# Performance work log

Measured on AMD Instinct MI355X. Metric: run time of the kernel, lower is better.

The kernel has to match this reference:

```python
import jax, jax.numpy as jnp
import numpy as np

NUM_CLASSES = 80
TOPK = 100
EPS = 1e-6


def _conv(x, w, b, pad):
    y = jax.lax.conv_general_dilated(
        x, w, window_strides=(1, 1), padding=[(pad, pad), (pad, pad)],
        dimension_numbers=('NCHW', 'OIHW', 'NCHW'))
    return y + b[None, :, None, None]


def _seek_local_maximum(p):
    # 8-neighbor local-maximum test with zero padding, plus >= EPS threshold.
    pp = jnp.pad(p, ((0, 0), (0, 0), (1, 1), (1, 1)))
    m = ((p >= pp[:, :, :-2, 1:-1]) & (p >= pp[:, :, 2:, 1:-1]) &
         (p >= pp[:, :, 1:-1, :-2]) & (p >= pp[:, :, 1:-1, 2:]) &
         (p >= pp[:, :, :-2, :-2]) & (p >= pp[:, :, :-2, 2:]) &
         (p >= pp[:, :, 2:, :-2]) & (p >= pp[:, :, 2:, 2:]) &
         (p >= EPS))
    return m.astype(p.dtype)


def setup_inputs() -> dict:
    key = jax.random.key(0)
    k = jax.random.split(key, 4)
    B, C, H, W = 8, 256, 128, 128
    return {
        'x': jax.random.normal(k[0], (B, C, H, W), jnp.float32),
        'pos_embeddings': jax.random.normal(k[1], (1, C, H, W), jnp.float32),
        'w1': jax.random.normal(k[2], (C, C, 3, 3), jnp.float32) * 0.02,
        'b1': jnp.zeros((C,), jnp.float32),
        'w2': jax.random.normal(k[3], (NUM_CLASSES + 1, C, 1, 1), jnp.float32) * 0.02,
        'b2': jnp.zeros((NUM_CLASSES + 1,), jnp.float32),
    }


def reference(x, pos_embeddings, w1, b1, w2, b2):
    b, c, h, w = x.shape
    # conv3x3 -> relu -> conv1x1 class logits  [b, num_classes+1, h, w]
    logits = _conv(jax.nn.relu(_conv(x, w1, b1, 1)), w2, b2, 0)
    probs = jax.nn.softmax(logits, axis=1)
    # keep only the winning foreground class per pixel (one-hot mask)
    cls_idx = jnp.argmax(probs[:, :NUM_CLASSES], axis=1)  # [b, h, w]
    one_hot = jax.nn.one_hot(cls_idx, NUM_CLASSES + 1, dtype=probs.dtype)
    probs = probs * jnp.transpose(one_hot, (0, 3, 1, 2))
    # boost local maxima (unrolled NMS) then topk over best-class score map
    probs = probs + _seek_local_maximum(probs)
    scores = jnp.max(probs[:, :NUM_CLASSES], axis=1).reshape(b, h * w)
    _, idx = jax.lax.top_k(scores, TOPK)  # [b, TOPK]
    topk_proposals = jnp.take_along_axis(
        x.reshape(b, c, h * w), idx[:, None, :], axis=2)
    pe = jnp.broadcast_to(pos_embeddings, (b,) + pos_embeddings.shape[1:])
    topk_pos_embeddings = jnp.take_along_axis(
        pe.reshape(b, -1, h * w), idx[:, None, :], axis=2)
    # eval mode: topk_locations is None in the original; omit it here
    return topk_proposals, topk_pos_embeddings, logits
```

## Files before the change

kernel.cpp:

```cpp
#include <hip/hip_runtime.h>
#include <cmath>

#define BATCH 8
#define CHN 256
#define HH 128
#define WW 128
#define HWSZ (HH*WW)
#define NCLS 81
#define NFG 80
#define KTOP 100
#define EPSV 1e-6f

typedef __attribute__((ext_vector_type(8))) short short8;
typedef __attribute__((ext_vector_type(4))) float f32x4;

__device__ __forceinline__ ushort f2bf(float f) {
    unsigned u = __float_as_uint(f);
    return (ushort)((u + 0x7FFFu + ((u >> 16) & 1u)) >> 16);
}
__device__ __forceinline__ float bf2f(ushort h) {
    return __uint_as_float(((unsigned)h) << 16);
}

__device__ __forceinline__ void gl16(const void* g, void* l) {
    __builtin_amdgcn_global_load_lds(
        (const __attribute__((address_space(1))) void*)g,
        (__attribute__((address_space(3))) void*)l, 16, 0, 0);
}

__global__ __launch_bounds__(256) void prep_x(
    const float* __restrict__ x, ushort* __restrict__ xh, ushort* __restrict__ xl)
{
    __shared__ float tile[32][CHN + 1];
    const int blk = blockIdx.x;
    const int q4 = blk & 3, h = (blk >> 2) & 127, b = blk >> 9;
    const int w0 = q4 << 5;
    const int t = threadIdx.x;
    const int px1 = t & 31, cq = t >> 5;

    const float* xb = x + ((size_t)b * CHN) * HWSZ + h * WW + w0;
#pragma unroll 4
    for (int i = 0; i < 32; ++i) {
        int c = i * 8 + cq;
        tile[px1][c] = xb[(size_t)c * HWSZ + px1];
    }
    __syncthreads();
    for (int i = 0; i < 4; ++i) {
        int u = i * 256 + t;
        int c8 = u & 31, px = u >> 5;
        short8 hv, lv;
#pragma unroll
        for (int j = 0; j < 8; ++j) {
            float f = tile[px][c8 * 8 + j];
            ushort hb = f2bf(f);
            hv[j] = (short)hb;
            lv[j] = (short)f2bf(f - bf2f(hb));
        }
        size_t addr = ((size_t)b * HWSZ + h * WW + w0 + px) * CHN + c8 * 8;
        *(short8*)(xh + addr) = hv;
        *(short8*)(xl + addr) = lv;
    }
}

__global__ __launch_bounds__(256) void prep_w(
    const float* __restrict__ w1, const float* __restrict__ w2,
    ushort* __restrict__ Bsw, ushort* __restrict__ w2sw)
{
    int i = blockIdx.x * 256 + threadIdx.x;
    if (i < 73728) {
        int tap  = i >> 13;
        int rem  = i & 8191;
        int kt   = rem >> 10;
        int rem2 = rem & 1023;
        int ntg  = rem2 >> 6;
        int lane = rem2 & 63;
        int oc   = ntg * 16 + (lane & 15);
        int ic0  = kt * 32 + (lane >> 4) * 8;
        size_t base = (size_t)(tap * 8 + kt) * 16384 + (size_t)ntg * 512 + lane * 8;
#pragma unroll
        for (int j = 0; j < 8; ++j) {
            float w  = w1[(size_t)oc * 2304 + (ic0 + j) * 9 + tap];
            ushort hb = f2bf(w);
            Bsw[base + j]        = hb;
            Bsw[base + 8192 + j] = f2bf(w - bf2f(hb));
        }
    } else {
        int j2 = i - 73728;
        int kt   = j2 / 768;
        int rem  = j2 - kt * 768;
        int spl  = rem / 384;
        int rem2 = rem - spl * 384;
        int ntg  = rem2 >> 6;
        int lane = rem2 & 63;
        int oc   = ntg * 16 + (lane & 15);
        int ic0  = kt * 32 + (lane >> 4) * 8;
        size_t base = (size_t)(kt * 12 + spl * 6 + ntg) * 512 + lane * 8;
#pragma unroll
        for (int j = 0; j < 8; ++j) {
            float w = (oc < NCLS) ? w2[(size_t)oc * CHN + ic0 + j] : 0.f;
            ushort hb = f2bf(w);
            w2sw[base + j] = spl ? f2bf(w - bf2f(hb)) : hb;
        }
    }
}

__global__ __launch_bounds__(256, 2) void conv3_pipe(
    const ushort* __restrict__ xh, const ushort* __restrict__ xl,
    const ushort* __restrict__ Bsw, const float* __restrict__ b1,
    float* __restrict__ y)
{
    __shared__ ushort A[3][2][132 * 32];

    const int blk  = blockIdx.x;
    const int b    = blk & 7;
    const int h    = blk >> 3;
    const int t    = threadIdx.x;
    const int lane = t & 63;
    const int w    = t >> 6;
    const int l15  = lane & 15;
    const int q    = lane >> 4;

    int colb[4], ldsu[4], basew[4];
#pragma unroll
    for (int r = 0; r < 4; ++r) {
        int e   = (r * 256 + t) & 511;
        int pxs = (e >> 2) + 1;
        int qq  = e & 3;
        int qs  = qq ^ ((pxs >> 1) & 3);
        colb[r]  = (pxs - 1) * CHN + qs * 8;
        ldsu[r]  = pxs * 32 + qq * 8;
        basew[r] = ((((r * 256 + (t & 192)) & 511) >> 2) + 1) * 32;
    }

    const short8 zz = {0, 0, 0, 0, 0, 0, 0, 0};
    f32x4 acc[8][4];
#pragma unroll
    for (int i = 0; i < 8; ++i)
#pragma unroll
        for (int j = 0; j < 4; ++j) { f32x4 z = {0.f, 0.f, 0.f, 0.f}; acc[i][j] = z; }

    if (t < 96) {
        int sl = t >> 5, rr = t & 31, arr = rr >> 4, pp = (rr >> 2) & 3, qq = rr & 3;
        int pxs = pp ? 128 + pp : 0;
        *(short8*)&A[sl][arr][pxs * 32 + qq * 8] = zz;
    }

    auto stage = [&](int sn) {
        int kt1 = sn / 3;
        int kh1 = sn - kt1 * 3;
        int gh  = h - 1 + kh1;
        if ((unsigned)gh < (unsigned)HH) {
            size_t rowb = ((size_t)(b * HH + gh) * WW) * CHN + kt1 * 32;
#pragma unroll
            for (int r = 0; r < 4; ++r) {
                const ushort* g = (r < 2 ? xh : xl) + rowb + colb[r];
                gl16(g, &A[kh1][r >> 1][basew[r]]);
            }
        } else {
#pragma unroll
            for (int r = 0; r < 4; ++r)
                *(short8*)&A[kh1][r >> 1][ldsu[r]] = zz;
        }
    };

    stage(0);
    __syncthreads();

#pragma unroll 1
    for (int s = 0; s < 24; ++s) {
        const int kt = s / 3;
        const int kh = s - kt * 3;
#pragma unroll
        for (int kw = 0; kw < 3; ++kw) {
            const int tap = kh * 3 + kw;
            const ushort* bk = Bsw + (size_t)(tap * 8 + kt) * 16384 + lane * 8;
            short8 bh[4], bl[4];
#pragma unroll
            for (int nt = 0; nt < 4; ++nt) {
                bh[nt] = *(const short8*)(bk + (w * 4 + nt) * 512);
                bl[nt] = *(const short8*)(bk + 8192 + (w * 4 + nt) * 512);
            }
            if (kw == 0 && s < 23) stage(s + 1);
#pragma unroll
            for (int mth = 0; mth < 8; mth += 4) {
                short8 ahf[4], alf[4];
#pragma unroll
                for (int mm = 0; mm < 4; ++mm) {
                    int pxs = (mth + mm) * 16 + l15 + kw;
                    int cof = pxs * 32 + ((q ^ ((pxs >> 1) & 3)) * 8);
                    ahf[mm] = *(const short8*)&A[kh][0][cof];
                    alf[mm] = *(const short8*)&A[kh][1][cof];
                }
                __builtin_amdgcn_s_setprio(1);
#pragma unroll
                for (int nt = 0; nt < 4; ++nt) {
#pragma unroll
                    for (int mm = 0; mm < 4; ++mm)
                        acc[mth + mm][nt] = __builtin_amdgcn_mfma_f32_16x16x32_bf16(
                            ahf[mm], bh[nt], acc[mth + mm][nt], 0, 0, 0);
#pragma unroll
                    for (int mm = 0; mm < 4; ++mm)
                        acc[mth + mm][nt] = __builtin_amdgcn_mfma_f32_16x16x32_bf16(
                            ahf[mm], bl[nt], acc[mth + mm][nt], 0, 0, 0);
#pragma unroll
                    for (int mm = 0; mm < 4; ++mm)
                        acc[mth + mm][nt] = __builtin_amdgcn_mfma_f32_16x16x32_bf16(
                            alf[mm], bh[nt], acc[mth + mm][nt], 0, 0, 0);
                }
                __builtin_amdgcn_s_setprio(0);
            }
        }
        __syncthreads();
    }

    const size_t rowbase = (size_t)b * HWSZ + h * WW;
#pragma unroll
    for (int nt = 0; nt < 4; ++nt) {
        const int oc = w * 64 + nt * 16 + l15;
        const float bias = b1[oc];
#pragma unroll
        for (int mt = 0; mt < 8; ++mt) {
#pragma unroll
            for (int r = 0; r < 4; ++r) {
                const int px = mt * 16 + q * 4 + r;
                float v = acc[mt][nt][r] + bias;
                y[(rowbase + px) * CHN + oc] = v > 0.f ? v : 0.f;
            }
        }
    }
}

__global__ __launch_bounds__(256) void head_mfma(
    const float* __restrict__ y, const ushort* __restrict__ w2sw,
    const float* __restrict__ b2, float* __restrict__ logits_out,
    int* __restrict__ cls_map, float* __restrict__ prob_map)
{
    __shared__ float ls[128][97];
    const int blk = blockIdx.x;
    const int b = blk >> 7, h = blk & 127;
    const int t = threadIdx.x, lane = t & 63, wm = t >> 6;
    const int l15 = lane & 15, q = lane >> 4;

    f32x4 acc[2][6];
#pragma unroll
    for (int i = 0; i < 2; ++i)
#pragma unroll
        for (int j = 0; j < 6; ++j) { f32x4 z = {0.f, 0.f, 0.f, 0.f}; acc[i][j] = z; }

    const size_t rowbase = (size_t)b * HWSZ + h * WW;

    for (int kt = 0; kt < 8; ++kt) {
        short8 ah[2], al[2];
#pragma unroll
        for (int mt = 0; mt < 2; ++mt) {
            const float* src = y + (rowbase + wm * 32 + mt * 16 + l15) * CHN + kt * 32 + q * 8;
            float4 f0 = *(const float4*)src;
            float4 f1 = *(const float4*)(src + 4);
            float fv[8] = {f0.x, f0.y, f0.z, f0.w, f1.x, f1.y, f1.z, f1.w};
#pragma unroll
            for (int j = 0; j < 8; ++j) {
                ushort hb = f2bf(fv[j]);
                ah[mt][j] = (short)hb;
                al[mt][j] = (short)f2bf(fv[j] - bf2f(hb));
            }
        }
        const ushort* bk = w2sw + (size_t)kt * 12 * 512 + lane * 8;
#pragma unroll
        for (int nt = 0; nt < 6; ++nt) {
            short8 bh = *(const short8*)(bk + nt * 512);
            short8 bl = *(const short8*)(bk + (6 + nt) * 512);
#pragma unroll
            for (int mt = 0; mt < 2; ++mt) {
                acc[mt][nt] = __builtin_amdgcn_mfma_f32_16x16x32_bf16(ah[mt], bh, acc[mt][nt], 0, 0, 0);
                acc[mt][nt] = __builtin_amdgcn_mfma_f32_16x16x32_bf16(ah[mt], bl, acc[mt][nt], 0, 0, 0);
                acc[mt][nt] = __builtin_amdgcn_mfma_f32_16x16x32_bf16(al[mt], bh, acc[mt][nt], 0, 0, 0);
            }
        }
    }

#pragma unroll
    for (int nt = 0; nt < 6; ++nt) {
        const int oc = nt * 16 + l15;
        const float bias = (oc < NCLS) ? b2[oc] : 0.f;
#pragma unroll
        for (int mt = 0; mt < 2; ++mt) {
#pragma unroll
            for (int r = 0; r < 4; ++r) {
                const int px = wm * 32 + mt * 16 + q * 4 + r;
                ls[px][oc] = acc[mt][nt][r] + bias;
            }
        }
    }
    __syncthreads();

    for (int i = t; i < NCLS * 128; i += 256) {
        int c = i >> 7, px = i & 127;
        logits_out[((size_t)b * NCLS + c) * HWSZ + h * WW + px] = ls[px][c];
    }

    if (t < 128) {
        const int px = t;
        float m = -1e30f;
#pragma unroll
        for (int c = 0; c < NCLS; ++c) m = fmaxf(m, ls[px][c]);
        float s = 0.f;
        for (int c = 0; c < NCLS; ++c) s += expf(ls[px][c] - m);
        float best = -1e30f; int bc = 0;
        for (int c = 0; c < NFG; ++c) {
            float v = ls[px][c];
            if (v > best) { best = v; bc = c; }
        }
        cls_map[rowbase + px]  = bc;
        prob_map[rowbase + px] = expf(best - m) / s;
    }
}

__global__ __launch_bounds__(256) void locmax_kernel(
    const int* __restrict__ cls_map, const float* __restrict__ prob_map,
    float* __restrict__ score)
{
    int i = blockIdx.x * 256 + threadIdx.x;
    int b = i >> 14;
    int p = i & (HWSZ - 1);
    int h = p >> 7, w = p & 127;
    int mycls = cls_map[i];
    float myp = prob_map[i];
    bool lm = (myp >= EPSV);
#pragma unroll
    for (int dh = -1; dh <= 1; ++dh)
#pragma unroll
        for (int dw = -1; dw <= 1; ++dw) {
            if (dh == 0 && dw == 0) continue;
            int nh = h + dh, nw = w + dw;
            if ((unsigned)nh < HH && (unsigned)nw < WW) {
                int ni = b * HWSZ + nh * WW + nw;
                if (cls_map[ni] == mycls && myp < prob_map[ni]) lm = false;
            }
        }
    score[i] = myp + (lm ? 1.f : 0.f);
}

__global__ __launch_bounds__(1024) void topk_kernel(
    const float* __restrict__ score, int* __restrict__ idx_out)
{
    __shared__ unsigned int hist[256];
    __shared__ unsigned long long cand[2048];
    __shared__ unsigned int sprefix, sneed, scntA, scntB;
    const int b = blockIdx.x;
    const int t = threadIdx.x;
    const float* sc = score + b * HWSZ;

    unsigned keys[16];
#pragma unroll
    for (int i = 0; i < 16; ++i)
        keys[i] = __float_as_uint(sc[t + (i << 10)]);

    if (t == 0) { sneed = KTOP; sprefix = 0; scntA = 0; scntB = 0; }

    for (int lvl = 0; lvl < 4; ++lvl) {
        const int shift = 24 - 8 * lvl;
        if (t < 256) hist[t] = 0;
        __syncthreads();
        const unsigned pref = sprefix;
#pragma unroll
        for (int i = 0; i < 16; ++i) {
            unsigned k = keys[i];
            bool match = (lvl == 0) || ((k >> (shift + 8)) == pref);
            if (match) atomicAdd(&hist[(k >> shift) & 255u], 1u);
        }
        __syncthreads();
        if (t == 0) {
            unsigned needv = sneed, c = 0; int bsel = 0;
            for (int j = 255; j >= 0; --j) {
                unsigned nc = c + hist[j];
                if (nc >= needv) { bsel = j; break; }
                c = nc;
            }
            sprefix = (pref << 8) | (unsigned)bsel;
            sneed = needv - c;
        }
        __syncthreads();
    }

    const unsigned K = sprefix;
#pragma unroll
    for (int i = 0; i < 16; ++i) {
        unsigned k = keys[i];
        int p = t + (i << 10);
        if (k > K) {
            unsigned pos = atomicAdd(&scntA, 1u);
            cand[pos] = ((unsigned long long)k << 32) | (unsigned)(~p);
        } else if (k == K) {
            unsigned pos = atomicAdd(&scntB, 1u);
            if (pos < 1920u)
                cand[128 + pos] = ((unsigned long long)k << 32) | (unsigned)(~p);
        }
    }
    __syncthreads();
    const int cA = (int)scntA;
    const int cB = (int)(scntB < 1920u ? scntB : 1920u);
    const int Ctot = cA + cB;
    for (int ti = t; ti < Ctot; ti += 1024) {
        unsigned long long my = cand[ti < cA ? ti : 128 + (ti - cA)];
        int rank = 0;
        for (int j = 0; j < Ctot; ++j) {
            unsigned long long o = cand[j < cA ? j : 128 + (j - cA)];
            rank += (o > my) ? 1 : 0;
        }
        if (rank < KTOP)
            idx_out[b * KTOP + rank] =
                (int)(~(unsigned)(my & 0xFFFFFFFFull)) & (HWSZ - 1);
    }
}

__global__ __launch_bounds__(256) void gather_kernel(
    const float* __restrict__ x, const float* __restrict__ pos,
    const int* __restrict__ idx, float* __restrict__ out0,
    float* __restrict__ out1)
{
    int blk = blockIdx.x;
    int b = blk / KTOP;
    int j = blk - b * KTOP;
    int c = threadIdx.x;
    int pix = idx[b * KTOP + j];
    out0[((size_t)b * CHN + c) * KTOP + j] = x[((size_t)b * CHN + c) * HWSZ + pix];
    out1[((size_t)b * CHN + c) * KTOP + j] = pos[(size_t)c * HWSZ + pix];
}

extern "C" void kernel_launch(void* const* d_in, const int* in_sizes, int n_in,
                              void* d_out, int out_size, void* d_ws, size_t ws_size,
                              hipStream_t stream) {
    (void)in_sizes; (void)n_in; (void)out_size; (void)ws_size;
    const float* x   = (const float*)d_in[0];
    const float* pos = (const float*)d_in[1];
    const float* w1  = (const float*)d_in[2];
    const float* b1  = (const float*)d_in[3];
    const float* w2  = (const float*)d_in[4];
    const float* b2  = (const float*)d_in[5];

    float* out0   = (float*)d_out;
    float* out1   = out0 + BATCH * CHN * KTOP;
    float* logits = out1 + BATCH * CHN * KTOP;

    char* ws = (char*)d_ws;
    const size_t NPX = (size_t)BATCH * HWSZ;

    size_t off = 0;
    int*    cls_map  = (int*)(ws + off);    off += NPX * 4;
    float*  prob_map = (float*)(ws + off);  off += NPX * 4;
    float*  score    = (float*)(ws + off);  off += NPX * 4;
    int*    idx      = (int*)(ws + off);    off += 4096;
    ushort* w2sw     = (ushort*)(ws + off); off += (size_t)8 * 12 * 512 * 2;
    ushort* Bsw      = (ushort*)(ws + off); off += (size_t)9 * 8 * 16384 * 2;
    ushort* xh       = (ushort*)(ws + off); off += NPX * CHN * 2;
    ushort* xl       = (ushort*)(ws + off); off += NPX * CHN * 2;
    float*  y        = (float*)(ws + off);  off += NPX * CHN * 4;

    prep_x<<<4096, 256, 0, stream>>>(x, xh, xl);
    prep_w<<<312, 256, 0, stream>>>(w1, w2, Bsw, w2sw);
    conv3_pipe<<<1024, 256, 0, stream>>>(xh, xl, Bsw, b1, y);
    head_mfma<<<1024, 256, 0, stream>>>(y, w2sw, b2, logits, cls_map, prob_map);
    locmax_kernel<<<(int)(NPX / 256), 256, 0, stream>>>(cls_map, prob_map, score);
    topk_kernel<<<BATCH, 1024, 0, stream>>>(score, idx);
    gather_kernel<<<BATCH * KTOP, 256, 0, stream>>>(x, pos, idx, out0, out1);
}
```

Baseline: 716.6 us.

## Fuse 1x1 class head and softmax epilogue into conv3x3 kernel

The conv3x3 kernel no longer writes the full fp32 ReLU activation tensor to global memory. It stages 32-pixel chunks of the accumulators into swizzled shared memory, reusing the input staging buffer through a union, and runs the 1x1 head MFMA, logits store and softmax/argmax there directly. This removes a 128 MB write and read-back plus one kernel launch. In exchange the conv epilogue gets longer, with extra block barriers and a larger LDS footprint that may limit occupancy.

```diff
diff --git a/kernel.cpp b/kernel.cpp
--- a/kernel.cpp
+++ b/kernel.cpp
@@ -26,6 +26,10 @@
     __builtin_amdgcn_global_load_lds(
         (const __attribute__((address_space(1))) void*)g,
         (__attribute__((address_space(3))) void*)l, 16, 0, 0);
+}
+
+__device__ __forceinline__ int ys_idx(int row, int col) {
+    return row * 256 + ((((col >> 2) ^ row) & 15) << 2) + ((col >> 2) & ~15) * 4 + (col & 3);
 }
 
 __global__ __launch_bounds__(256) void prep_x(
@@ -104,12 +108,17 @@
     }
 }
 
-__global__ __launch_bounds__(256, 2) void conv3_pipe(
+__global__ __launch_bounds__(256, 2) void conv3_fused(
     const ushort* __restrict__ xh, const ushort* __restrict__ xl,
     const ushort* __restrict__ Bsw, const float* __restrict__ b1,
-    float* __restrict__ y)
-{
-    __shared__ ushort A[3][2][132 * 32];
+    const ushort* __restrict__ w2sw, const float* __restrict__ b2,
+    float* __restrict__ logits_out, int* __restrict__ cls_map,
+    float* __restrict__ prob_map)
+{
+    __shared__ union SMU {
+        ushort A[3][2][132 * 32];
+        struct { float ys[32 * 256]; float ls[32 * 103]; } ep;
+    } sm;
 
     const int blk  = blockIdx.x;
     const int b    = blk & 7;
@@ -142,7 +151,7 @@
     if (t < 96) {
         int sl = t >> 5, rr = t & 31, arr = rr >> 4, pp = (rr >> 2) & 3, qq = rr & 3;
         int pxs = pp ? 128 + pp : 0;
-        *(short8*)&A[sl][arr][pxs * 32 + qq * 8] = zz;
+        *(short8*)&sm.A[sl][arr][pxs * 32 + qq * 8] = zz;
     }
 
     auto stage = [&](int sn) {
@@ -154,12 +163,12 @@
 #pragma unroll
             for (int r = 0; r < 4; ++r) {
                 const ushort* g = (r < 2 ? xh : xl) + rowb + colb[r];
-                gl16(g, &A[kh1][r >> 1][basew[r]]);
+                gl16(g, &sm.A[kh1][r >> 1][basew[r]]);
             }
         } else {
 #pragma unroll
             for (int r = 0; r < 4; ++r)
-                *(short8*)&A[kh1][r >> 1][ldsu[r]] = zz;
+                *(short8*)&sm.A[kh1][r >> 1][ldsu[r]] = zz;
         }
     };
 
@@ -188,8 +197,8 @@
                 for (int mm = 0; mm < 4; ++mm) {
                     int pxs = (mth + mm) * 16 + l15 + kw;
                     int cof = pxs * 32 + ((q ^ ((pxs >> 1) & 3)) * 8);
-                    ahf[mm] = *(const short8*)&A[kh][0][cof];
-                    alf[mm] = *(const short8*)&A[kh][1][cof];
+                    ahf[mm] = *(const short8*)&sm.A[kh][0][cof];
+                    alf[mm] = *(const short8*)&sm.A[kh][1][cof];
                 }
                 __builtin_amdgcn_s_setprio(1);
 #pragma unroll
@@ -214,104 +223,95 @@
     }
 
     const size_t rowbase = (size_t)b * HWSZ + h * WW;
-#pragma unroll
-    for (int nt = 0; nt < 4; ++nt) {
-        const int oc = w * 64 + nt * 16 + l15;
-        const float bias = b1[oc];
-#pragma unroll
-        for (int mt = 0; mt < 8; ++mt) {
-#pragma unroll
-            for (int r = 0; r < 4; ++r) {
-                const int px = mt * 16 + q * 4 + r;
-                float v = acc[mt][nt][r] + bias;
-                y[(rowbase + px) * CHN + oc] = v > 0.f ? v : 0.f;
-            }
-        }
-    }
-}
-
-__global__ __launch_bounds__(256) void head_mfma(
-    const float* __restrict__ y, const ushort* __restrict__ w2sw,
-    const float* __restrict__ b2, float* __restrict__ logits_out,
-    int* __restrict__ cls_map, float* __restrict__ prob_map)
-{
-    __shared__ float ls[128][97];
-    const int blk = blockIdx.x;
-    const int b = blk >> 7, h = blk & 127;
-    const int t = threadIdx.x, lane = t & 63, wm = t >> 6;
-    const int l15 = lane & 15, q = lane >> 4;
-
-    f32x4 acc[2][6];
-#pragma unroll
-    for (int i = 0; i < 2; ++i)
-#pragma unroll
-        for (int j = 0; j < 6; ++j) { f32x4 z = {0.f, 0.f, 0.f, 0.f}; acc[i][j] = z; }
-
-    const size_t rowbase = (size_t)b * HWSZ + h * WW;
-
-    for (int kt = 0; kt < 8; ++kt) {
-        short8 ah[2], al[2];
-#pragma unroll
-        for (int mt = 0; mt < 2; ++mt) {
-            const float* src = y + (rowbase + wm * 32 + mt * 16 + l15) * CHN + kt * 32 + q * 8;
-            float4 f0 = *(const float4*)src;
-            float4 f1 = *(const float4*)(src + 4);
+    const int mt2sel = w >> 1;
+    const int ntb    = (w & 1) * 3;
+
+    float b1c[4];
+#pragma unroll
+    for (int nt = 0; nt < 4; ++nt) b1c[nt] = b1[w * 64 + nt * 16 + l15];
+    float b2c[3];
+#pragma unroll
+    for (int j = 0; j < 3; ++j) {
+        int oc2 = (ntb + j) * 16 + l15;
+        b2c[j] = (oc2 < NCLS) ? b2[oc2] : 0.f;
+    }
+
+    float* ys = sm.ep.ys;
+    float* ls = sm.ep.ls;
+
+#pragma unroll
+    for (int p = 0; p < 4; ++p) {
+        __syncthreads();
+#pragma unroll
+        for (int h2 = 0; h2 < 2; ++h2) {
+#pragma unroll
+            for (int nt = 0; nt < 4; ++nt) {
+                const int col = w * 64 + nt * 16 + l15;
+#pragma unroll
+                for (int r = 0; r < 4; ++r) {
+                    const int row = h2 * 16 + q * 4 + r;
+                    float v = acc[2 * p + h2][nt][r] + b1c[nt];
+                    ys[ys_idx(row, col)] = v > 0.f ? v : 0.f;
+                }
+            }
+        }
+        __syncthreads();
+        f32x4 acc2[3];
+#pragma unroll
+        for (int j = 0; j < 3; ++j) { f32x4 z = {0.f, 0.f, 0.f, 0.f}; acc2[j] = z; }
+        const int arow = mt2sel * 16 + l15;
+#pragma unroll
+        for (int kt = 0; kt < 8; ++kt) {
+            const int c0 = kt * 32 + q * 8;
+            float4 f0 = *(const float4*)&ys[arow * 256 + ((((c0 >> 2) ^ arow) & 15) << 2) + ((c0 >> 2) & ~15) * 4];
+            const int c1 = c0 + 4;
+            float4 f1 = *(const float4*)&ys[arow * 256 + ((((c1 >> 2) ^ arow) & 15) << 2) + ((c1 >> 2) & ~15) * 4];
             float fv[8] = {f0.x, f0.y, f0.z, f0.w, f1.x, f1.y, f1.z, f1.w};
+            short8 ah, al;
 #pragma unroll
             for (int j = 0; j < 8; ++j) {
                 ushort hb = f2bf(fv[j]);
-                ah[mt][j] = (short)hb;
-                al[mt][j] = (short)f2bf(fv[j] - bf2f(hb));
-            }
-        }
-        const ushort* bk = w2sw + (size_t)kt * 12 * 512 + lane * 8;
-#pragma unroll
-        for (int nt = 0; nt < 6; ++nt) {
-            short8 bh = *(const short8*)(bk + nt * 512);
-            short8 bl = *(const short8*)(bk + (6 + nt) * 512);
-#pragma unroll
-            for (int mt = 0; mt < 2; ++mt) {
-                acc[mt][nt] = __builtin_amdgcn_mfma_f32_16x16x32_bf16(ah[mt], bh, acc[mt][nt], 0, 0, 0);
-                acc[mt][nt] = __builtin_amdgcn_mfma_f32_16x16x32_bf16(ah[mt], bl, acc[mt][nt], 0, 0, 0);
-                acc[mt][nt] = __builtin_amdgcn_mfma_f32_16x16x32_bf16(al[mt], bh, acc[mt][nt], 0, 0, 0);
-            }
-        }
-    }
-
-#pragma unroll
-    for (int nt = 0; nt < 6; ++nt) {
-        const int oc = nt * 16 + l15;
-        const float bias = (oc < NCLS) ? b2[oc] : 0.f;
-#pragma unroll
-        for (int mt = 0; mt < 2; ++mt) {
-#pragma unroll
-            for (int r = 0; r < 4; ++r) {
-                const int px = wm * 32 + mt * 16 + q * 4 + r;
-                ls[px][oc] = acc[mt][nt][r] + bias;
-            }
-        }
-    }
-    __syncthreads();
-
-    for (int i = t; i < NCLS * 128; i += 256) {
-        int c = i >> 7, px = i & 127;
-        logits_out[((size_t)b * NCLS + c) * HWSZ + h * WW + px] = ls[px][c];
-    }
-
-    if (t < 128) {
-        const int px = t;
-        float m = -1e30f;
-#pragma unroll
-        for (int c = 0; c < NCLS; ++c) m = fmaxf(m, ls[px][c]);
-        float s = 0.f;
-        for (int c = 0; c < NCLS; ++c) s += expf(ls[px][c] - m);
-        float best = -1e30f; int bc = 0;
-        for (int c = 0; c < NFG; ++c) {
-            float v = ls[px][c];
-            if (v > best) { best = v; bc = c; }
-        }
-        cls_map[rowbase + px]  = bc;
-        prob_map[rowbase + px] = expf(best - m) / s;
+                ah[j] = (short)hb;
+                al[j] = (short)f2bf(fv[j] - bf2f(hb));
+            }
+            const ushort* bk = w2sw + (size_t)kt * 12 * 512 + lane * 8;
+#pragma unroll
+            for (int j = 0; j < 3; ++j) {
+                const int nt = ntb + j;
+                short8 bh = *(const short8*)(bk + nt * 512);
+                short8 bl = *(const short8*)(bk + (6 + nt) * 512);
+                acc2[j] = __builtin_amdgcn_mfma_f32_16x16x32_bf16(ah, bh, acc2[j], 0, 0, 0);
+                acc2[j] = __builtin_amdgcn_mfma_f32_16x16x32_bf16(ah, bl, acc2[j], 0, 0, 0);
+                acc2[j] = __builtin_amdgcn_mfma_f32_16x16x32_bf16(al, bh, acc2[j], 0, 0, 0);
+            }
+        }
+#pragma unroll
+        for (int j = 0; j < 3; ++j) {
+            const int oc2 = (ntb + j) * 16 + l15;
+#pragma unroll
+            for (int r = 0; r < 4; ++r)
+                ls[(mt2sel * 16 + q * 4 + r) * 103 + oc2] = acc2[j][r] + b2c[j];
+        }
+        __syncthreads();
+        if (t < 32) {
+            const int px = t;
+            float m = -1e30f;
+#pragma unroll
+            for (int c = 0; c < NCLS; ++c) m = fmaxf(m, ls[px * 103 + c]);
+            float s = 0.f;
+            for (int c = 0; c < NCLS; ++c) s += expf(ls[px * 103 + c] - m);
+            float best = -1e30f; int bc = 0;
+            for (int c = 0; c < NFG; ++c) {
+                float v = ls[px * 103 + c];
+                if (v > best) { best = v; bc = c; }
+            }
+            cls_map[rowbase + p * 32 + px]  = bc;
+            prob_map[rowbase + p * 32 + px] = expf(best - m) / s;
+        }
+        for (int i = t; i < NCLS * 32; i += 256) {
+            int c = i >> 5, pxl = i & 31;
+            logits_out[((size_t)b * NCLS + c) * HWSZ + h * WW + p * 32 + pxl] = ls[pxl * 103 + c];
+        }
     }
 }
 
@@ -454,12 +454,11 @@
     ushort* Bsw      = (ushort*)(ws + off); off += (size_t)9 * 8 * 16384 * 2;
     ushort* xh       = (ushort*)(ws + off); off += NPX * CHN * 2;
     ushort* xl       = (ushort*)(ws + off); off += NPX * CHN * 2;
-    float*  y        = (float*)(ws + off);  off += NPX * CHN * 4;
 
     prep_x<<<4096, 256, 0, stream>>>(x, xh, xl);
     prep_w<<<312, 256, 0, stream>>>(w1, w2, Bsw, w2sw);
-    conv3_pipe<<<1024, 256, 0, stream>>>(xh, xl, Bsw, b1, y);
-    head_mfma<<<1024, 256, 0, stream>>>(y, w2sw, b2, logits, cls_map, prob_map);
+    conv3_fused<<<1024, 256, 0, stream>>>(xh, xl, Bsw, b1, w2sw, b2,
+                                          logits, cls_map, prob_map);
     locmax_kernel<<<(int)(NPX / 256), 256, 0, stream>>>(cls_map, prob_map, score);
     topk_kernel<<<BATCH, 1024, 0, stream>>>(score, idx);
     gather_kernel<<<BATCH * KTOP, 256, 0, stream>>>(x, pos, idx, out0, out1);
```

Result: slower. 760.2 us (+6.1%).

## Deepen conv3 staging pipeline, prefetch head inputs, and re-pad transpose tile

Applied to the files above, without the earlier changes.

In the 3x3 conv kernel, input rows are now staged two steps ahead instead of one. The per-step __syncthreads is replaced by an explicit vmcnt wait plus s_barrier, and the boundary-row zero fills move to a one-time prologue. In the head kernel, all y fragments are software-prefetched into registers and refilled ahead of use. The prep_x LDS tile gets a padded layout (stride 10 per 8 channels) to reduce bank conflicts. The hand-written waitcnt counts are fragile and must match the number of async loads issued per stage, and the prefetch buffers add register pressure.

```diff
diff --git a/kernel.cpp b/kernel.cpp
--- a/kernel.cpp
+++ b/kernel.cpp
@@ -31,7 +31,7 @@
 __global__ __launch_bounds__(256) void prep_x(
     const float* __restrict__ x, ushort* __restrict__ xh, ushort* __restrict__ xl)
 {
-    __shared__ float tile[32][CHN + 1];
+    __shared__ float tile[32 * 321];
     const int blk = blockIdx.x;
     const int q4 = blk & 3, h = (blk >> 2) & 127, b = blk >> 9;
     const int w0 = q4 << 5;
@@ -41,8 +41,7 @@
     const float* xb = x + ((size_t)b * CHN) * HWSZ + h * WW + w0;
 #pragma unroll 4
     for (int i = 0; i < 32; ++i) {
-        int c = i * 8 + cq;
-        tile[px1][c] = xb[(size_t)c * HWSZ + px1];
+        tile[px1 * 321 + i * 10 + cq] = xb[(size_t)(i * 8 + cq) * HWSZ + px1];
     }
     __syncthreads();
     for (int i = 0; i < 4; ++i) {
@@ -51,7 +50,7 @@
         short8 hv, lv;
 #pragma unroll
         for (int j = 0; j < 8; ++j) {
-            float f = tile[px][c8 * 8 + j];
+            float f = tile[px * 321 + c8 * 10 + j];
             ushort hb = f2bf(f);
             hv[j] = (short)hb;
             lv[j] = (short)f2bf(f - bf2f(hb));
@@ -120,7 +119,7 @@
     const int l15  = lane & 15;
     const int q    = lane >> 4;
 
-    int colb[4], ldsu[4], basew[4];
+    int colb[4], basew[4];
 #pragma unroll
     for (int r = 0; r < 4; ++r) {
         int e   = (r * 256 + t) & 511;
@@ -128,7 +127,6 @@
         int qq  = e & 3;
         int qs  = qq ^ ((pxs >> 1) & 3);
         colb[r]  = (pxs - 1) * CHN + qs * 8;
-        ldsu[r]  = pxs * 32 + qq * 8;
         basew[r] = ((((r * 256 + (t & 192)) & 511) >> 2) + 1) * 32;
     }
 
@@ -143,6 +141,13 @@
         int sl = t >> 5, rr = t & 31, arr = rr >> 4, pp = (rr >> 2) & 3, qq = rr & 3;
         int pxs = pp ? 128 + pp : 0;
         *(short8*)&A[sl][arr][pxs * 32 + qq * 8] = zz;
+    }
+    if (h == 0 || h == 127) {
+        const int sl = (h == 0) ? 0 : 2;
+        for (int u = t; u < 1056; u += 256) {
+            int arr = u >= 528; int v = arr ? u - 528 : u;
+            *(short8*)&A[sl][arr][v * 8] = zz;
+        }
     }
 
     auto stage = [&](int sn) {
@@ -156,20 +161,25 @@
                 const ushort* g = (r < 2 ? xh : xl) + rowb + colb[r];
                 gl16(g, &A[kh1][r >> 1][basew[r]]);
             }
-        } else {
-#pragma unroll
-            for (int r = 0; r < 4; ++r)
-                *(short8*)&A[kh1][r >> 1][ldsu[r]] = zz;
         }
     };
 
     stage(0);
-    __syncthreads();
+    stage(1);
 
 #pragma unroll 1
     for (int s = 0; s < 24; ++s) {
         const int kt = s / 3;
         const int kh = s - kt * 3;
+        {
+            const int kh1n = (s + 1) % 3;
+            const bool nx4 = (s < 23) &&
+                !((h == 0 && kh1n == 0) || (h == 127 && kh1n == 2));
+            if (nx4) asm volatile("s_waitcnt vmcnt(4) lgkmcnt(0)" ::: "memory");
+            else     asm volatile("s_waitcnt vmcnt(0) lgkmcnt(0)" ::: "memory");
+            __builtin_amdgcn_s_barrier();
+            __builtin_amdgcn_sched_barrier(0);
+        }
 #pragma unroll
         for (int kw = 0; kw < 3; ++kw) {
             const int tap = kh * 3 + kw;
@@ -180,7 +190,7 @@
                 bh[nt] = *(const short8*)(bk + (w * 4 + nt) * 512);
                 bl[nt] = *(const short8*)(bk + 8192 + (w * 4 + nt) * 512);
             }
-            if (kw == 0 && s < 23) stage(s + 1);
+            if (kw == 0 && s < 22) stage(s + 2);
 #pragma unroll
             for (int mth = 0; mth < 8; mth += 4) {
                 short8 ahf[4], alf[4];
@@ -210,7 +220,6 @@
                 __builtin_amdgcn_s_setprio(0);
             }
         }
-        __syncthreads();
     }
 
     const size_t rowbase = (size_t)b * HWSZ + h * WW;
@@ -248,14 +257,26 @@
         for (int j = 0; j < 6; ++j) { f32x4 z = {0.f, 0.f, 0.f, 0.f}; acc[i][j] = z; }
 
     const size_t rowbase = (size_t)b * HWSZ + h * WW;
-
+    const float* yb0 = y + (rowbase + wm * 32 + l15) * CHN + q * 8;
+    const float* yb1 = yb0 + 16 * CHN;
+
+    float4 fa[2][4], fb[2][4];
+#pragma unroll
+    for (int k = 0; k < 4; ++k) {
+        fa[0][k] = *(const float4*)(yb0 + k * 32);
+        fb[0][k] = *(const float4*)(yb0 + k * 32 + 4);
+        fa[1][k] = *(const float4*)(yb1 + k * 32);
+        fb[1][k] = *(const float4*)(yb1 + k * 32 + 4);
+    }
+
+#pragma unroll
     for (int kt = 0; kt < 8; ++kt) {
+        const int sl = kt & 3;
         short8 ah[2], al[2];
 #pragma unroll
         for (int mt = 0; mt < 2; ++mt) {
-            const float* src = y + (rowbase + wm * 32 + mt * 16 + l15) * CHN + kt * 32 + q * 8;
-            float4 f0 = *(const float4*)src;
-            float4 f1 = *(const float4*)(src + 4);
+            float4 f0 = fa[mt][sl];
+            float4 f1 = fb[mt][sl];
             float fv[8] = {f0.x, f0.y, f0.z, f0.w, f1.x, f1.y, f1.z, f1.w};
 #pragma unroll
             for (int j = 0; j < 8; ++j) {
@@ -263,6 +284,12 @@
                 ah[mt][j] = (short)hb;
                 al[mt][j] = (short)f2bf(fv[j] - bf2f(hb));
             }
+        }
+        if (kt < 4) {
+            fa[0][sl] = *(const float4*)(yb0 + (kt + 4) * 32);
+            fb[0][sl] = *(const float4*)(yb0 + (kt + 4) * 32 + 4);
+            fa[1][sl] = *(const float4*)(yb1 + (kt + 4) * 32);
+            fb[1][sl] = *(const float4*)(yb1 + (kt + 4) * 32 + 4);
         }
         const ushort* bk = w2sw + (size_t)kt * 12 * 512 + lane * 8;
 #pragma unroll
```

Measured after the change: 702.6 us. About the same (-2.0%).
